# Performance work log

Hardware: AMD Instinct MI355X
Metric: run time of the kernel (lower is better)

Reference implementation:

```python
import jax, jax.numpy as jnp
import numpy as np

N = 50000
SELF_LOOP_W = 2.0  # GCNConv(improved=True)


def gcn_conv(x, edge_index, W, b):
    # x: [N, Fin], edge_index: [2, E] (row=source, col=target)
    h = x @ W  # [N, Fout]
    row, col = edge_index[0], edge_index[1]
    ones = jnp.ones(row.shape[0], dtype=h.dtype)
    deg = jax.ops.segment_sum(ones, col, num_segments=N) + SELF_LOOP_W
    dinv = jnp.where(deg > 0, jax.lax.rsqrt(deg), 0.0)
    norm = dinv[row] * dinv[col]  # [E]
    agg = jax.ops.segment_sum(norm[:, None] * h[row], col, num_segments=N)
    # self-loop contribution: weight 2.0, norm = dinv[i]^2
    agg = agg + (SELF_LOOP_W * dinv * dinv)[:, None] * h
    return agg + b


def setup_inputs() -> dict:
    key = jax.random.key(0)
    ks = jax.random.split(key, 12)
    F_in, H1, H2, H3 = 256, 256, 128, 64
    E, Ep, En = 800000, 200000, 200000
    def glorot(k, shape):
        lim = np.sqrt(6.0 / (shape[0] + shape[1]))
        return jax.random.uniform(k, shape, jnp.float32, -lim, lim)
    return {
        "x": jax.random.normal(ks[0], (N, F_in), jnp.float32),
        "train_edge_index": jax.random.randint(ks[1], (2, E), 0, N),
        "pos_edge_index": jax.random.randint(ks[2], (2, Ep), 0, N),
        "neg_edge_index": jax.random.randint(ks[3], (2, En), 0, N),
        "W1": glorot(ks[4], (F_in, H1)),
        "b1": jnp.zeros((H1,), jnp.float32),
        "W2": glorot(ks[5], (H1, H2)),
        "b2": jnp.zeros((H2,), jnp.float32),
        "Wl1": glorot(ks[6], (H2, H3)),
        "bl1": jnp.zeros((H3,), jnp.float32),
        "Wl2": glorot(ks[7], (H3, 1)),
        "bl2": jnp.zeros((1,), jnp.float32),
    }


def reference(x, train_edge_index, pos_edge_index, neg_edge_index,
              W1, b1, W2, b2, Wl1, bl1, Wl2, bl2):
    h = jax.nn.relu(gcn_conv(x, train_edge_index, W1, b1))
    h = gcn_conv(h, train_edge_index, W2, b2)  # [N, 128]
    tei = jnp.concatenate([pos_edge_index, neg_edge_index], axis=-1)  # [2, Ep+En]
    e = h[tei[1]] + h[tei[0]]  # x_i + x_j, [Etot, 128]
    e = jax.nn.relu(e @ Wl1 + bl1)
    e = jax.nn.sigmoid(e @ Wl2 + bl2)
    return e.reshape(-1)
```

## Files before the change

kernel.cpp:

```cpp
#include <hip/hip_runtime.h>
#include <math.h>

#define NV 50000
#define ETR 800000
#define EPOS 200000
#define ETEST 400000

typedef __attribute__((ext_vector_type(8))) short bf16x8;
typedef __attribute__((ext_vector_type(8))) unsigned short ushortx8;
typedef __attribute__((ext_vector_type(4))) float f32x4;

__device__ inline unsigned short f2b(float f) {
    union { float f; unsigned u; } v; v.f = f;
    unsigned r = v.u + 0x7fffu + ((v.u >> 16) & 1u);
    return (unsigned short)(r >> 16);
}
__device__ inline float blo(unsigned q) { union { unsigned u; float f; } v; v.u = q << 16; return v.f; }
__device__ inline float bhi(unsigned q) { union { unsigned u; float f; } v; v.u = q & 0xffff0000u; return v.f; }
__device__ inline float b2f(unsigned short s) { union { unsigned u; float f; } v; v.u = ((unsigned)s) << 16; return v.f; }

__device__ inline ushortx8 bf16add8(ushortx8 a, ushortx8 b) {
    ushortx8 r;
    #pragma unroll
    for (int i = 0; i < 8; ++i)
        r[i] = f2b(b2f(a[i]) + b2f(b[i]));
    return r;
}


template<int N, int K, bool AF32>
__device__ __forceinline__ void gemm_body(
    const void* __restrict__ Av, const unsigned short* __restrict__ Bt,
    unsigned short* __restrict__ C, int M, int row0, int col0)
{
    constexpr int BK = 64;
    __shared__ unsigned short smem[18464];
    unsigned short (*Asm)[BK] = (unsigned short (*)[BK])smem;
    unsigned short (*Bsm)[BK] = (unsigned short (*)[BK])(smem + 8192);
    int tid = threadIdx.x;
    int lane = tid & 63, wid = tid >> 6;
    int wr = wid >> 1, wc = wid & 1;

    int sr = tid >> 3;
    int s8 = tid & 7;
    int sswz = s8 ^ (sr & 7);
    int fr = lane & 15;
    int g  = lane >> 4;

    f32x4 acc[4][4] = {};

    for (int k0 = 0; k0 < K; k0 += BK) {
        #pragma unroll
        for (int i = 0; i < 4; ++i) {
            int r = sr + i * 32;
            int gr = row0 + r;
            ushortx8 va = {0, 0, 0, 0, 0, 0, 0, 0};
            if constexpr (AF32) {
                const float* Af = (const float*)Av;
                if (gr < M) {
                    float4 f0 = *(const float4*)&Af[(size_t)gr * K + k0 + s8 * 8];
                    float4 f1 = *(const float4*)&Af[(size_t)gr * K + k0 + s8 * 8 + 4];
                    va[0] = f2b(f0.x); va[1] = f2b(f0.y); va[2] = f2b(f0.z); va[3] = f2b(f0.w);
                    va[4] = f2b(f1.x); va[5] = f2b(f1.y); va[6] = f2b(f1.z); va[7] = f2b(f1.w);
                }
            } else {
                const unsigned short* Ab = (const unsigned short*)Av;
                if (gr < M) va = *(const ushortx8*)&Ab[(size_t)gr * K + k0 + s8 * 8];
            }
            *(ushortx8*)&Asm[r][sswz * 8] = va;
            ushortx8 vb = *(const ushortx8*)&Bt[(size_t)(col0 + r) * K + k0 + s8 * 8];
            *(ushortx8*)&Bsm[r][sswz * 8] = vb;
        }
        __syncthreads();
        #pragma unroll
        for (int kf = 0; kf < BK; kf += 32) {
            int sbase = kf >> 3;
            bf16x8 af[4], bfr[4];
            #pragma unroll
            for (int m = 0; m < 4; ++m) {
                int rr = wr * 64 + m * 16 + fr;
                af[m] = *(const bf16x8*)&Asm[rr][((sbase + g) ^ (fr & 7)) * 8];
            }
            #pragma unroll
            for (int n = 0; n < 4; ++n) {
                int rr = wc * 64 + n * 16 + fr;
                bfr[n] = *(const bf16x8*)&Bsm[rr][((sbase + g) ^ (fr & 7)) * 8];
            }
            #pragma unroll
            for (int m = 0; m < 4; ++m)
                #pragma unroll
                for (int n = 0; n < 4; ++n)
                    acc[m][n] = __builtin_amdgcn_mfma_f32_16x16x32_bf16(af[m], bfr[n], acc[m][n], 0, 0, 0);
        }
        __syncthreads();
    }

    {
        unsigned short* cw = smem + wid * 4616;
        #pragma unroll
        for (int m = 0; m < 4; ++m)
            #pragma unroll
            for (int n = 0; n < 4; ++n)
                #pragma unroll
                for (int j = 0; j < 4; ++j)
                    cw[(m * 16 + g * 4 + j) * 72 + n * 16 + fr] = f2b(acc[m][n][j]);
        __syncthreads();
        int row = tid >> 1;
        int half = tid & 1;
        int q = ((row >> 6) << 1) + half;
        int rl = row & 63;
        const unsigned short* cr = smem + q * 4616 + rl * 72;
        int gr = row0 + row;
        if (gr < M) {
            unsigned short* gp = C + (size_t)gr * N + col0 + half * 64;
            #pragma unroll
            for (int c8 = 0; c8 < 8; ++c8)
                *(ushortx8*)&gp[c8 * 8] = *(const ushortx8*)&cr[c8 * 8];
        }
    }
}


__global__ __launch_bounds__(256) void fat0_kernel(
    const int* __restrict__ tei, int* __restrict__ deg,
    const float* __restrict__ W1, unsigned short* __restrict__ w1t)
{
    int bid = blockIdx.x;
    int t = threadIdx.x;
    if (bid < 3125) {
        int e = bid * 256 + t;
        if (e < ETR) atomicAdd(&deg[tei[ETR + e]], 1);
    } else {
        int i = (bid - 3125) * 256 + t;
        w1t[i] = f2b(W1[(i & 255) * 256 + (i >> 8)]);
    }
}


__global__ __launch_bounds__(256) void fat1_kernel(
    const float* __restrict__ x, const unsigned short* __restrict__ w1t,
    unsigned short* __restrict__ h1lin,
    const int* __restrict__ deg, int* __restrict__ partials,
    const float* __restrict__ W2, unsigned short* __restrict__ w2t,
    const float* __restrict__ Wl1, unsigned short* __restrict__ wl1t)
{
    int bid = blockIdx.x;
    int t = threadIdx.x;
    if (bid < 782) {
        int row0 = (bid >> 1) * 128, col0 = (bid & 1) * 128;
        gemm_body<256, 256, true>(x, w1t, h1lin, NV, row0, col0);
    } else if (bid < 831) {
        int p = bid - 782;
        int base = p * 1024;
        int s = 0;
        #pragma unroll
        for (int k = 0; k < 4; ++k) {
            int i = base + t + k * 256;
            if (i < NV) s += deg[i];
        }
        #pragma unroll
        for (int off = 32; off > 0; off >>= 1) s += __shfl_xor(s, off);
        __shared__ int ws4[4];
        if ((t & 63) == 0) ws4[t >> 6] = s;
        __syncthreads();
        if (t == 0) partials[p] = ws4[0] + ws4[1] + ws4[2] + ws4[3];
    } else if (bid < 959) {
        int i = (bid - 831) * 256 + t;
        w2t[i] = f2b(W2[(i & 255) * 128 + (i >> 8)]);
    } else {
        int i = (bid - 959) * 256 + t;
        wl1t[i] = f2b(Wl1[(i & 127) * 64 + (i >> 7)]);
    }
}


__global__ __launch_bounds__(1024) void ptr_kernel(
    const int* __restrict__ deg, const int* __restrict__ partials,
    int* __restrict__ ptr, int* __restrict__ cursor, float* __restrict__ dinv)
{
    int b = blockIdx.x, t = threadIdx.x;
    int i = b * 1024 + t;
    int d = (i < NV) ? deg[i] : 0;
    int lane = t & 63, w = t >> 6;
    int v = d;
    #pragma unroll
    for (int off = 1; off < 64; off <<= 1) {
        int u = __shfl_up(v, off);
        if (lane >= off) v += u;
    }
    __shared__ int wsum[16], woff[16];
    if (lane == 63) wsum[w] = v;
    __syncthreads();
    if (t == 0) {
        int s = 0;
        for (int k = 0; k < b; ++k) s += partials[k];
        for (int k = 0; k < 16; ++k) { woff[k] = s; s += wsum[k]; }
    }
    __syncthreads();
    int excl = woff[w] + v - d;
    if (i < NV) {
        ptr[i] = excl;
        cursor[i] = excl;
        dinv[i] = rsqrtf((float)d + 2.0f);
        if (i == NV - 1) ptr[NV] = excl + d;
    }
}

__global__ void fill_kernel(const int* __restrict__ tei, const float* __restrict__ dinv,
                            int* __restrict__ cursor, int2* __restrict__ edat) {
    int e = blockIdx.x * blockDim.x + threadIdx.x;
    if (e < ETR) {
        int row = tei[e];
        int col = tei[ETR + e];
        int p = atomicAdd(&cursor[col], 1);
        edat[p] = make_int2(row, __float_as_int(dinv[row] * dinv[col]));
    }
}


__global__ __launch_bounds__(256) void gemm2_kernel(
    const unsigned short* __restrict__ A, const unsigned short* __restrict__ Bt,
    unsigned short* __restrict__ C)
{
    gemm_body<128, 256, false>(A, Bt, C, NV, blockIdx.x * 128, 0);
}


template<int F, bool RELU>
__global__ __launch_bounds__(256) void gather_kernel(
    const int* __restrict__ ptr, const int2* __restrict__ edat,
    const float* __restrict__ dinv, const unsigned short* __restrict__ hlin,
    const float* __restrict__ bias, unsigned short* __restrict__ hout)
{
    constexpr int V = F / 64;
    int gid = blockIdx.x * blockDim.x + threadIdx.x;
    int node = gid >> 6, lane = gid & 63;
    if (node >= NV) return;
    float dc = dinv[node];
    int j0 = ptr[node], j1 = ptr[node + 1];
    float acc[V] = {};
    const unsigned short* hb = hlin + lane * V;
    const long long* edl = (const long long*)edat;

    int j = j0;
    for (; j + 7 < j1; j += 8) {
        long long e[8];
        #pragma unroll
        for (int u = 0; u < 8; ++u) e[u] = __builtin_nontemporal_load(edl + j + u);
        if constexpr (V == 4) {
            uint2 q[8];
            #pragma unroll
            for (int u = 0; u < 8; ++u)
                q[u] = *(const uint2*)(hb + (size_t)(int)e[u] * F);
            #pragma unroll
            for (int u = 0; u < 8; ++u) {
                float n = __int_as_float((int)(e[u] >> 32));
                acc[0] += n * blo(q[u].x);
                acc[1] += n * bhi(q[u].x);
                acc[2] += n * blo(q[u].y);
                acc[3] += n * bhi(q[u].y);
            }
        } else {
            unsigned q[8];
            #pragma unroll
            for (int u = 0; u < 8; ++u)
                q[u] = *(const unsigned*)(hb + (size_t)(int)e[u] * F);
            #pragma unroll
            for (int u = 0; u < 8; ++u) {
                float n = __int_as_float((int)(e[u] >> 32));
                acc[0] += n * blo(q[u]);
                acc[1] += n * bhi(q[u]);
            }
        }
    }
    for (; j + 3 < j1; j += 4) {
        long long e[4];
        #pragma unroll
        for (int u = 0; u < 4; ++u) e[u] = __builtin_nontemporal_load(edl + j + u);
        if constexpr (V == 4) {
            uint2 q[4];
            #pragma unroll
            for (int u = 0; u < 4; ++u)
                q[u] = *(const uint2*)(hb + (size_t)(int)e[u] * F);
            #pragma unroll
            for (int u = 0; u < 4; ++u) {
                float n = __int_as_float((int)(e[u] >> 32));
                acc[0] += n * blo(q[u].x);
                acc[1] += n * bhi(q[u].x);
                acc[2] += n * blo(q[u].y);
                acc[3] += n * bhi(q[u].y);
            }
        } else {
            unsigned q[4];
            #pragma unroll
            for (int u = 0; u < 4; ++u)
                q[u] = *(const unsigned*)(hb + (size_t)(int)e[u] * F);
            #pragma unroll
            for (int u = 0; u < 4; ++u) {
                float n = __int_as_float((int)(e[u] >> 32));
                acc[0] += n * blo(q[u]);
                acc[1] += n * bhi(q[u]);
            }
        }
    }
    for (; j < j1; ++j) {
        long long e0 = __builtin_nontemporal_load(edl + j);
        float n0 = __int_as_float((int)(e0 >> 32));
        if constexpr (V == 4) {
            uint2 q0 = *(const uint2*)(hb + (size_t)(int)e0 * F);
            acc[0] += n0 * blo(q0.x);
            acc[1] += n0 * bhi(q0.x);
            acc[2] += n0 * blo(q0.y);
            acc[3] += n0 * bhi(q0.y);
        } else {
            unsigned q0 = *(const unsigned*)(hb + (size_t)(int)e0 * F);
            acc[0] += n0 * blo(q0);
            acc[1] += n0 * bhi(q0);
        }
    }

    const unsigned short* ps = hb + (size_t)node * F;
    float sw = 2.0f * dc * dc;
    if constexpr (V == 4) {
        uint2 qs = *(const uint2*)ps;
        float o0 = acc[0] + sw * blo(qs.x) + bias[lane * 4 + 0];
        float o1 = acc[1] + sw * bhi(qs.x) + bias[lane * 4 + 1];
        float o2 = acc[2] + sw * blo(qs.y) + bias[lane * 4 + 2];
        float o3 = acc[3] + sw * bhi(qs.y) + bias[lane * 4 + 3];
        if (RELU) {
            o0 = fmaxf(o0, 0.f); o1 = fmaxf(o1, 0.f);
            o2 = fmaxf(o2, 0.f); o3 = fmaxf(o3, 0.f);
        }
        union { unsigned short u[4]; unsigned long long ll; } pk;
        pk.u[0] = f2b(o0); pk.u[1] = f2b(o1); pk.u[2] = f2b(o2); pk.u[3] = f2b(o3);
        __builtin_nontemporal_store(pk.ll, (unsigned long long*)(hout + (size_t)node * F + lane * 4));
    } else {
        unsigned qs = *(const unsigned*)ps;
        float o0 = acc[0] + sw * blo(qs) + bias[lane * 2 + 0];
        float o1 = acc[1] + sw * bhi(qs) + bias[lane * 2 + 1];
        if (RELU) { o0 = fmaxf(o0, 0.f); o1 = fmaxf(o1, 0.f); }
        union { unsigned short u[2]; unsigned q; } pk;
        pk.u[0] = f2b(o0); pk.u[1] = f2b(o1);
        __builtin_nontemporal_store(pk.q, (unsigned*)(hout + (size_t)node * F + lane * 2));
    }
}


__global__ __launch_bounds__(256) void edge_mlp_mfma_kernel(
    const int* __restrict__ pos, const int* __restrict__ neg,
    const unsigned short* __restrict__ h2, const unsigned short* __restrict__ Wl1t,
    const float* __restrict__ bl1, const float* __restrict__ Wl2,
    const float* __restrict__ bl2, float* __restrict__ out)
{
    __shared__ unsigned short Es[128][128];
    __shared__ unsigned short Ws[64][128];
    int tid = threadIdx.x;
    int lane = tid & 63, w = tid >> 6;
    int fr = lane & 15, g = lane >> 4;
    int e0 = blockIdx.x * 128;

    #pragma unroll
    for (int k = 0; k < 4; ++k) {
        int chunk = tid + k * 256;
        int row = chunk >> 4, c = chunk & 15;
        *(ushortx8*)&Ws[row][(c ^ (row & 7)) * 8] = *(const ushortx8*)&Wl1t[chunk * 8];
    }

    int et = tid >> 1, hh = tid & 1;
    int eg = e0 + et;
    int a, b;
    if (eg < EPOS) { a = pos[eg]; b = pos[EPOS + eg]; }
    else { int i = eg - EPOS; a = neg[i]; b = neg[EPOS + i]; }
    const unsigned short* pa = h2 + (size_t)a * 128 + hh * 64;
    const unsigned short* pb = h2 + (size_t)b * 128 + hh * 64;
    #pragma unroll
    for (int c8 = 0; c8 < 8; ++c8) {
        ushortx8 va = *(const ushortx8*)&pa[c8 * 8];
        ushortx8 vb = *(const ushortx8*)&pb[c8 * 8];
        ushortx8 vs = bf16add8(va, vb);
        int c = hh * 8 + c8;
        *(ushortx8*)&Es[et][(c ^ (et & 7)) * 8] = vs;
    }
    __syncthreads();

    f32x4 acc[2][4] = {};
    #pragma unroll
    for (int ks = 0; ks < 4; ++ks) {
        int c = ks * 4 + g;
        bf16x8 af[2], bfr[4];
        #pragma unroll
        for (int m = 0; m < 2; ++m) {
            int r = w * 32 + m * 16 + fr;
            af[m] = *(const bf16x8*)&Es[r][(c ^ (r & 7)) * 8];
        }
        #pragma unroll
        for (int n = 0; n < 4; ++n) {
            int r = n * 16 + fr;
            bfr[n] = *(const bf16x8*)&Ws[r][(c ^ (r & 7)) * 8];
        }
        #pragma unroll
        for (int m = 0; m < 2; ++m)
            #pragma unroll
            for (int n = 0; n < 4; ++n)
                acc[m][n] = __builtin_amdgcn_mfma_f32_16x16x32_bf16(af[m], bfr[n], acc[m][n], 0, 0, 0);
    }

    float bl2v = bl2[0];
    float b1v[4], w2v[4];
    #pragma unroll
    for (int n = 0; n < 4; ++n) {
        b1v[n] = bl1[n * 16 + fr];
        w2v[n] = Wl2[n * 16 + fr];
    }
    #pragma unroll
    for (int m = 0; m < 2; ++m) {
        float p[4];
        #pragma unroll
        for (int j = 0; j < 4; ++j) {
            float s = 0.f;
            #pragma unroll
            for (int n = 0; n < 4; ++n)
                s += fmaxf(acc[m][n][j] + b1v[n], 0.0f) * w2v[n];
            p[j] = s;
        }
        #pragma unroll
        for (int off = 1; off < 16; off <<= 1) {
            #pragma unroll
            for (int j = 0; j < 4; ++j)
                p[j] += __shfl_xor(p[j], off);
        }
        int ebase = e0 + w * 32 + m * 16 + g * 4;
        #pragma unroll
        for (int j = 0; j < 4; ++j)
            if (fr == j)
                out[ebase + j] = 1.0f / (1.0f + expf(-(p[j] + bl2v)));
    }
}


extern "C" void kernel_launch(void* const* d_in, const int* in_sizes, int n_in,
                              void* d_out, int out_size, void* d_ws, size_t ws_size,
                              hipStream_t stream) {
    const float* x   = (const float*)d_in[0];
    const int*   tei = (const int*)d_in[1];
    const int*   pos = (const int*)d_in[2];
    const int*   neg = (const int*)d_in[3];
    const float* W1  = (const float*)d_in[4];
    const float* b1  = (const float*)d_in[5];
    const float* W2  = (const float*)d_in[6];
    const float* b2  = (const float*)d_in[7];
    const float* Wl1 = (const float*)d_in[8];
    const float* bl1 = (const float*)d_in[9];
    const float* Wl2 = (const float*)d_in[10];
    const float* bl2 = (const float*)d_in[11];
    float* out = (float*)d_out;

    float* fws = (float*)d_ws;
    int*   iws = (int*)d_ws;
    unsigned short* usws = (unsigned short*)d_ws;
    float* dinv     = fws;
    int*   deg      = iws + 50000;
    int*   ptr      = iws + 100000;
    int*   cursor   = iws + 150002;
    int2*  edat     = (int2*)(iws + 200064);
    int*   partials = iws + 1800064;
    unsigned short* w1t  = usws + 2ull * 1800192;
    unsigned short* w2t  = usws + 2ull * 1832960;
    unsigned short* wl1t = usws + 2ull * 1849344;
    unsigned short* bufX = usws + 2ull * 1853504;
    unsigned short* bufL16 = usws + 2ull * 8253504;
    unsigned short* bufH = usws + 2ull * 14653504;

    hipMemsetAsync(deg, 0, NV * sizeof(int), stream);

    fat0_kernel<<<3381, 256, 0, stream>>>(tei, deg, W1, w1t);

    fat1_kernel<<<991, 256, 0, stream>>>(x, w1t, bufL16, deg, partials, W2, w2t, Wl1, wl1t);

    ptr_kernel<<<49, 1024, 0, stream>>>(deg, partials, ptr, cursor, dinv);
    fill_kernel<<<(ETR + 255) / 256, 256, 0, stream>>>(tei, dinv, cursor, edat);

    gather_kernel<256, true><<<(NV * 64) / 256, 256, 0, stream>>>(ptr, edat, dinv, bufL16, b1, bufH);

    gemm2_kernel<<<391, 256, 0, stream>>>(bufH, w2t, bufX);
    gather_kernel<128, false><<<(NV * 64) / 256, 256, 0, stream>>>(ptr, edat, dinv, bufX, b2, bufL16);

    edge_mlp_mfma_kernel<<<ETEST / 128, 256, 0, stream>>>(pos, neg, bufL16, wl1t, bl1, Wl2, bl2, out);
}
```

Before: 289.3 us.

## Fuse CSR fill into GEMM1 launch, self-contained prefix scan, direct-to-LDS loads

The degree-partials step is removed. The ptr kernel now computes each block's prefix base by summing all earlier degrees itself, so it can run before the first GEMM. The edge-fill scatter then moves into the same launch as the x@W1 GEMM, so the atomic scatter can overlap the matmul and one launch disappears. Separately, GEMM tile staging for B, and for A when it is bf16, uses global_load_lds to write global data straight into LDS with the swizzle applied to the source address. The redundant prefix sums in ptr2 cost extra reads of deg, which grow with block index.

```diff
diff --git a/kernel.cpp b/kernel.cpp
--- a/kernel.cpp
+++ b/kernel.cpp
@@ -26,6 +26,10 @@
         r[i] = f2b(b2f(a[i]) + b2f(b[i]));
     return r;
 }
+
+#define GLOAD_LDS16(g, l) __builtin_amdgcn_global_load_lds( \
+    (__attribute__((address_space(1))) void*)(g), \
+    (__attribute__((address_space(3))) void*)(l), 16, 0, 0)
 
 
 template<int N, int K, bool AF32>
@@ -43,7 +47,6 @@
 
     int sr = tid >> 3;
     int s8 = tid & 7;
-    int sswz = s8 ^ (sr & 7);
     int fr = lane & 15;
     int g  = lane >> 4;
 
@@ -54,22 +57,22 @@
         for (int i = 0; i < 4; ++i) {
             int r = sr + i * 32;
             int gr = row0 + r;
-            ushortx8 va = {0, 0, 0, 0, 0, 0, 0, 0};
+            int s8sw = s8 ^ (r & 7);
+            GLOAD_LDS16(&Bt[(size_t)(col0 + r) * K + k0 + s8sw * 8], &Bsm[r][s8 * 8]);
             if constexpr (AF32) {
                 const float* Af = (const float*)Av;
+                ushortx8 va = {0, 0, 0, 0, 0, 0, 0, 0};
                 if (gr < M) {
                     float4 f0 = *(const float4*)&Af[(size_t)gr * K + k0 + s8 * 8];
                     float4 f1 = *(const float4*)&Af[(size_t)gr * K + k0 + s8 * 8 + 4];
                     va[0] = f2b(f0.x); va[1] = f2b(f0.y); va[2] = f2b(f0.z); va[3] = f2b(f0.w);
                     va[4] = f2b(f1.x); va[5] = f2b(f1.y); va[6] = f2b(f1.z); va[7] = f2b(f1.w);
                 }
+                *(ushortx8*)&Asm[r][(s8 ^ (r & 7)) * 8] = va;
             } else {
                 const unsigned short* Ab = (const unsigned short*)Av;
-                if (gr < M) va = *(const ushortx8*)&Ab[(size_t)gr * K + k0 + s8 * 8];
-            }
-            *(ushortx8*)&Asm[r][sswz * 8] = va;
-            ushortx8 vb = *(const ushortx8*)&Bt[(size_t)(col0 + r) * K + k0 + s8 * 8];
-            *(ushortx8*)&Bsm[r][sswz * 8] = vb;
+                GLOAD_LDS16(&Ab[(size_t)gr * K + k0 + s8sw * 8], &Asm[r][s8 * 8]);
+            }
         }
         __syncthreads();
         #pragma unroll
@@ -137,63 +140,42 @@
 }
 
 
-__global__ __launch_bounds__(256) void fat1_kernel(
-    const float* __restrict__ x, const unsigned short* __restrict__ w1t,
-    unsigned short* __restrict__ h1lin,
-    const int* __restrict__ deg, int* __restrict__ partials,
-    const float* __restrict__ W2, unsigned short* __restrict__ w2t,
-    const float* __restrict__ Wl1, unsigned short* __restrict__ wl1t)
-{
-    int bid = blockIdx.x;
-    int t = threadIdx.x;
-    if (bid < 782) {
-        int row0 = (bid >> 1) * 128, col0 = (bid & 1) * 128;
-        gemm_body<256, 256, true>(x, w1t, h1lin, NV, row0, col0);
-    } else if (bid < 831) {
-        int p = bid - 782;
-        int base = p * 1024;
+__global__ __launch_bounds__(1024) void ptr2_kernel(
+    const int* __restrict__ deg, int* __restrict__ ptr,
+    int* __restrict__ cursor, float* __restrict__ dinv)
+{
+    int b = blockIdx.x, t = threadIdx.x;
+    int lane = t & 63, w = t >> 6;
+    __shared__ int wred[16], wsum[16], woff[16];
+    __shared__ int base_s;
+
+    int pre = 0;
+    int lim = b * 1024;
+    for (int i = t; i < lim; i += 1024) pre += deg[i];
+    #pragma unroll
+    for (int off = 32; off > 0; off >>= 1) pre += __shfl_xor(pre, off);
+    if (lane == 0) wred[w] = pre;
+    __syncthreads();
+    if (t == 0) {
         int s = 0;
         #pragma unroll
-        for (int k = 0; k < 4; ++k) {
-            int i = base + t + k * 256;
-            if (i < NV) s += deg[i];
-        }
-        #pragma unroll
-        for (int off = 32; off > 0; off >>= 1) s += __shfl_xor(s, off);
-        __shared__ int ws4[4];
-        if ((t & 63) == 0) ws4[t >> 6] = s;
-        __syncthreads();
-        if (t == 0) partials[p] = ws4[0] + ws4[1] + ws4[2] + ws4[3];
-    } else if (bid < 959) {
-        int i = (bid - 831) * 256 + t;
-        w2t[i] = f2b(W2[(i & 255) * 128 + (i >> 8)]);
-    } else {
-        int i = (bid - 959) * 256 + t;
-        wl1t[i] = f2b(Wl1[(i & 127) * 64 + (i >> 7)]);
-    }
-}
-
-
-__global__ __launch_bounds__(1024) void ptr_kernel(
-    const int* __restrict__ deg, const int* __restrict__ partials,
-    int* __restrict__ ptr, int* __restrict__ cursor, float* __restrict__ dinv)
-{
-    int b = blockIdx.x, t = threadIdx.x;
+        for (int k = 0; k < 16; ++k) s += wred[k];
+        base_s = s;
+    }
+
     int i = b * 1024 + t;
     int d = (i < NV) ? deg[i] : 0;
-    int lane = t & 63, w = t >> 6;
     int v = d;
     #pragma unroll
     for (int off = 1; off < 64; off <<= 1) {
         int u = __shfl_up(v, off);
         if (lane >= off) v += u;
     }
-    __shared__ int wsum[16], woff[16];
     if (lane == 63) wsum[w] = v;
     __syncthreads();
     if (t == 0) {
-        int s = 0;
-        for (int k = 0; k < b; ++k) s += partials[k];
+        int s = base_s;
+        #pragma unroll
         for (int k = 0; k < 16; ++k) { woff[k] = s; s += wsum[k]; }
     }
     __syncthreads();
@@ -206,14 +188,34 @@
     }
 }
 
-__global__ void fill_kernel(const int* __restrict__ tei, const float* __restrict__ dinv,
-                            int* __restrict__ cursor, int2* __restrict__ edat) {
-    int e = blockIdx.x * blockDim.x + threadIdx.x;
-    if (e < ETR) {
-        int row = tei[e];
-        int col = tei[ETR + e];
-        int p = atomicAdd(&cursor[col], 1);
-        edat[p] = make_int2(row, __float_as_int(dinv[row] * dinv[col]));
+
+__global__ __launch_bounds__(256) void fat1_kernel(
+    const float* __restrict__ x, const unsigned short* __restrict__ w1t,
+    unsigned short* __restrict__ h1lin,
+    const int* __restrict__ tei, const float* __restrict__ dinv,
+    int* __restrict__ cursor, int2* __restrict__ edat,
+    const float* __restrict__ W2, unsigned short* __restrict__ w2t,
+    const float* __restrict__ Wl1, unsigned short* __restrict__ wl1t)
+{
+    int bid = blockIdx.x;
+    int t = threadIdx.x;
+    if (bid < 782) {
+        int row0 = (bid >> 1) * 128, col0 = (bid & 1) * 128;
+        gemm_body<256, 256, true>(x, w1t, h1lin, NV, row0, col0);
+    } else if (bid < 3907) {
+        int e = (bid - 782) * 256 + t;
+        if (e < ETR) {
+            int row = tei[e];
+            int col = tei[ETR + e];
+            int p = atomicAdd(&cursor[col], 1);
+            edat[p] = make_int2(row, __float_as_int(dinv[row] * dinv[col]));
+        }
+    } else if (bid < 4035) {
+        int i = (bid - 3907) * 256 + t;
+        w2t[i] = f2b(W2[(i & 255) * 128 + (i >> 8)]);
+    } else {
+        int i = (bid - 4035) * 256 + t;
+        wl1t[i] = f2b(Wl1[(i & 127) * 64 + (i >> 7)]);
     }
 }
 
@@ -463,7 +465,6 @@
     int*   ptr      = iws + 100000;
     int*   cursor   = iws + 150002;
     int2*  edat     = (int2*)(iws + 200064);
-    int*   partials = iws + 1800064;
     unsigned short* w1t  = usws + 2ull * 1800192;
     unsigned short* w2t  = usws + 2ull * 1832960;
     unsigned short* wl1t = usws + 2ull * 1849344;
@@ -475,10 +476,10 @@
 
     fat0_kernel<<<3381, 256, 0, stream>>>(tei, deg, W1, w1t);
 
-    fat1_kernel<<<991, 256, 0, stream>>>(x, w1t, bufL16, deg, partials, W2, w2t, Wl1, wl1t);
-
-    ptr_kernel<<<49, 1024, 0, stream>>>(deg, partials, ptr, cursor, dinv);
-    fill_kernel<<<(ETR + 255) / 256, 256, 0, stream>>>(tei, dinv, cursor, edat);
+    ptr2_kernel<<<49, 1024, 0, stream>>>(deg, ptr, cursor, dinv);
+
+    fat1_kernel<<<4067, 256, 0, stream>>>(x, w1t, bufL16, tei, dinv, cursor, edat,
+                                          W2, w2t, Wl1, wl1t);
 
     gather_kernel<256, true><<<(NV * 64) / 256, 256, 0, stream>>>(ptr, edat, dinv, bufL16, b1, bufH);
 
```

Measured after the change: 281.3 us. 1.03x faster.
